# Kernel optimization log

Measured on AMD Instinct MI355X. Metric: run time of the kernel, lower is better.

Reference implementation:

```python
import jax, jax.numpy as jnp
import numpy as np

B, T, C, R = 4, 2048, 2048, 256


def setup_inputs() -> dict:
    key = jax.random.key(0)
    ks = jax.random.split(key, 12)
    s = 0.02
    return {
        "x": jax.random.normal(ks[0], (B, T, C), dtype=jnp.float32),
        "h_state": jnp.zeros((B, C), dtype=jnp.float32),
        "ln_gamma": jnp.ones((C,), dtype=jnp.float32),
        "ln_beta": jnp.zeros((C,), dtype=jnp.float32),
        "wq_a": jax.random.normal(ks[1], (C, R), dtype=jnp.float32) * s,
        "wq_b": jax.random.normal(ks[2], (R, C), dtype=jnp.float32) * s,
        "wk_a": jax.random.normal(ks[3], (C, R), dtype=jnp.float32) * s,
        "wk_b": jax.random.normal(ks[4], (R, C), dtype=jnp.float32) * s,
        "wv_a": jax.random.normal(ks[5], (C, R), dtype=jnp.float32) * s,
        "wv_b": jax.random.normal(ks[6], (R, C), dtype=jnp.float32) * s,
        "out_w": jax.random.normal(ks[7], (C, C), dtype=jnp.float32) * s,
        "out_b": jnp.zeros((C,), dtype=jnp.float32),
        "time_decay": jnp.full((C,), -0.5, dtype=jnp.float32),
    }


def _layernorm(x, gamma, beta, eps=1e-5):
    mu = jnp.mean(x, axis=-1, keepdims=True)
    var = jnp.var(x, axis=-1, keepdims=True)
    return (x - mu) * jax.lax.rsqrt(var + eps) * gamma + beta


def reference(x, h_state, ln_gamma, ln_beta, wq_a, wq_b, wk_a, wk_b, wv_a, wv_b, out_w, out_b, time_decay):
    b, t, c = x.shape
    xn = _layernorm(x, ln_gamma, ln_beta)
    # token shift: mix current with previous token
    x_shift = jnp.concatenate([jnp.zeros((b, 1, c), xn.dtype), xn[:, :-1, :]], axis=1)
    mix = 0.5 * xn + 0.5 * x_shift
    # low-rank projections: (B,T,C) @ (C,R) @ (R,C)
    q = jnp.einsum('btc,cr,rd->btd', mix, wq_a, wq_b)
    k = jnp.einsum('btc,cr,rd->btd', mix, wk_a, wk_b)
    v = jnp.einsum('btc,cr,rd->btd', mix, wv_a, wv_b)
    decay = jnp.exp(-jnp.exp(time_decay))  # (C,)

    kv = (k * v).transpose(1, 0, 2)          # (T,B,C)
    sq = jax.nn.sigmoid(q).transpose(1, 0, 2)  # (T,B,C)

    def step(h, inp):
        kv_t, sq_t = inp
        h = decay * h + kv_t
        return h, sq_t * h

    h_final, ys = jax.lax.scan(step, h_state, (kv, sq))
    out = ys.transpose(1, 0, 2)               # (B,T,C)
    out = jnp.einsum('btc,dc->btd', out, out_w) + out_b
    return out, h_final
```

## Files before the change

### kernel.cpp

```cpp
#include <hip/hip_runtime.h>


typedef __attribute__((ext_vector_type(8))) __bf16 bf16x8;
typedef __attribute__((ext_vector_type(4))) float f32x4;

static constexpr int Bb = 4, Tt = 2048, Cc = 2048, Rr = 256;
static constexpr int Mrows = Bb * Tt;
static constexpr int NCH = 32, CLEN = 64;

__device__ __forceinline__ unsigned short f2bf(float f) {
  union { float f; unsigned u; } a; a.f = f;
  unsigned r = (a.u + 0x7FFFu + ((a.u >> 16) & 1u)) >> 16;
  return (unsigned short)r;
}
__device__ __forceinline__ float bf2f(unsigned short h) {
  union { unsigned u; float f; } a; a.u = ((unsigned)h) << 16;
  return a.f;
}

__device__ __forceinline__ void gload16(const void* g, void* l) {
  __builtin_amdgcn_global_load_lds(
      (const __attribute__((address_space(1))) void*)g,
      (__attribute__((address_space(3))) void*)l, 16, 0, 0);
}

__global__ void prep_weights(const float* __restrict__ wqa, const float* __restrict__ wka,
                             const float* __restrict__ wva, const float* __restrict__ wqb,
                             const float* __restrict__ wkb, const float* __restrict__ wvb,
                             const float* __restrict__ ow,  const float* __restrict__ td,
                             unsigned short* __restrict__ waT, unsigned short* __restrict__ wbT,
                             unsigned short* __restrict__ owT, float* __restrict__ decay,
                             float* __restrict__ decayL) {
  const int g = blockIdx.x * blockDim.x + threadIdx.x;
  const int stride = gridDim.x * blockDim.x;
  for (int i = g; i < 3 * Rr * Cc; i += stride) {
    int c = i & (Cc - 1); int jj = i >> 11; int p = jj >> 8; int r = jj & (Rr - 1);
    const float* w = (p == 0) ? wqa : ((p == 1) ? wka : wva);
    waT[i] = f2bf(w[(size_t)c * Rr + r]);
  }
  for (int i = g; i < 3 * Cc * Rr; i += stride) {
    int r = i & (Rr - 1); int d = (i >> 8) & (Cc - 1); int p = i >> 19;
    const float* w = (p == 0) ? wqb : ((p == 1) ? wkb : wvb);
    wbT[i] = f2bf(w[(size_t)r * Cc + d]);
  }
  for (int i = g; i < Cc * Cc; i += stride) owT[i] = f2bf(ow[i]);
  for (int i = g; i < Cc; i += stride) {
    float e = expf(td[i]);
    decay[i] = expf(-e);
    decayL[i] = expf(-(float)CLEN * e);
  }
}

__global__ __launch_bounds__(256) void lnmix_kernel(
    const float* __restrict__ x, const float* __restrict__ gamma,
    const float* __restrict__ beta, unsigned short* __restrict__ mix) {
  const int m = blockIdx.x;
  const int t = m & (Tt - 1);
  const float* xr = x + (size_t)m * Cc;
  float s0 = 0.f, q0 = 0.f, s1 = 0.f, q1 = 0.f;
  float4 cur[2], prv[2];
#pragma unroll
  for (int r = 0; r < 2; ++r) {
    int i = threadIdx.x + r * 256;
    float4 v = ((const float4*)xr)[i];
    cur[r] = v;
    s0 += v.x + v.y + v.z + v.w;
    q0 += v.x * v.x + v.y * v.y + v.z * v.z + v.w * v.w;
  }
  if (t > 0) {
    const float* xp = xr - Cc;
#pragma unroll
    for (int r = 0; r < 2; ++r) {
      int i = threadIdx.x + r * 256;
      float4 v = ((const float4*)xp)[i];
      prv[r] = v;
      s1 += v.x + v.y + v.z + v.w;
      q1 += v.x * v.x + v.y * v.y + v.z * v.z + v.w * v.w;
    }
  }
#pragma unroll
  for (int off = 32; off; off >>= 1) {
    s0 += __shfl_down(s0, off); q0 += __shfl_down(q0, off);
    s1 += __shfl_down(s1, off); q1 += __shfl_down(q1, off);
  }
  __shared__ float red[4][4];
  __shared__ float bc[4];
  if ((threadIdx.x & 63) == 0) {
    int w = threadIdx.x >> 6;
    red[w][0] = s0; red[w][1] = q0; red[w][2] = s1; red[w][3] = q1;
  }
  __syncthreads();
  if (threadIdx.x == 0) {
    float a0 = 0, b0 = 0, a1 = 0, b1 = 0;
    for (int w = 0; w < 4; ++w) { a0 += red[w][0]; b0 += red[w][1]; a1 += red[w][2]; b1 += red[w][3]; }
    float mu0 = a0 * (1.f / Cc);
    bc[0] = mu0; bc[1] = rsqrtf(b0 * (1.f / Cc) - mu0 * mu0 + 1e-5f);
    float mu1 = a1 * (1.f / Cc);
    bc[2] = mu1; bc[3] = rsqrtf(b1 * (1.f / Cc) - mu1 * mu1 + 1e-5f);
  }
  __syncthreads();
  const float mu0 = bc[0], rs0 = bc[1], mu1 = bc[2], rs1 = bc[3];
#pragma unroll
  for (int r = 0; r < 2; ++r) {
    int i = threadIdx.x + r * 256;
    float4 g = ((const float4*)gamma)[i];
    float4 bb = ((const float4*)beta)[i];
    float4 v = cur[r];
    float mx = (v.x - mu0) * rs0 * g.x + bb.x;
    float my = (v.y - mu0) * rs0 * g.y + bb.y;
    float mz = (v.z - mu0) * rs0 * g.z + bb.z;
    float mw = (v.w - mu0) * rs0 * g.w + bb.w;
    if (t > 0) {
      float4 u = prv[r];
      mx = 0.5f * (mx + (u.x - mu1) * rs1 * g.x + bb.x);
      my = 0.5f * (my + (u.y - mu1) * rs1 * g.y + bb.y);
      mz = 0.5f * (mz + (u.z - mu1) * rs1 * g.z + bb.z);
      mw = 0.5f * (mw + (u.w - mu1) * rs1 * g.w + bb.w);
    } else {
      mx *= 0.5f; my *= 0.5f; mz *= 0.5f; mw *= 0.5f;
    }
    ushort4 o;
    o.x = f2bf(mx); o.y = f2bf(my); o.z = f2bf(mz); o.w = f2bf(mw);
    ((ushort4*)mix)[(size_t)m * 512 + i] = o;
  }
}

template <bool STORE_BF16, bool ADD_BIAS>
__global__ __launch_bounds__(512, 2) void gemm_pipe(
    const unsigned short* __restrict__ A0p, long lda, long aStrideP,
    const unsigned short* __restrict__ B0p, long ldb, long bStrideP,
    void* c0, void* c1, void* c2, long ldc, int K,
    const float* __restrict__ bias, int nbx, int nby) {
  __shared__ unsigned short lds[4 * 16384];
  const int tid = threadIdx.x;
  const int nwg = gridDim.x;
  const int id = blockIdx.x;
  const int q = nwg >> 3;
  const int swz = (id & 7) * q + (id >> 3);
  const int per = nbx * nby;
  const int p = swz / per;
  const int r2 = swz - p * per;
  const int mblk = r2 / nbx;
  const int nblk = r2 - mblk * nbx;
  const unsigned short* A  = A0p + (long)p * aStrideP;
  const unsigned short* Bt = B0p + (long)p * bStrideP;
  void* Cout = (p == 0) ? c0 : (p == 1 ? c1 : c2);
  const long m0 = (long)mblk * 256, n0 = (long)nblk * 256;

  const int lane = tid & 63, wid = tid >> 6;
  const int wm = wid >> 2, wn = wid & 3;
  const int fr = lane & 15, fq = lane >> 4;

  const int srow = tid >> 2;
  const int s_src = (tid & 3) ^ ((tid >> 3) & 3);
  const unsigned short* Ag = A + (m0 + srow) * lda + s_src * 8;
  const unsigned short* Bg = Bt + (n0 + srow) * ldb + s_src * 8;

  const int swzs = fq ^ ((fr >> 1) & 3);
  const unsigned short* aBase = &lds[(wm * 128 + fr) * 32 + swzs * 8];
  const unsigned short* bBase = &lds[8192 + (wn * 64 + fr) * 32 + swzs * 8];

  f32x4 acc[8][4];
#pragma unroll
  for (int i = 0; i < 8; ++i)
#pragma unroll
    for (int j = 0; j < 4; ++j) acc[i][j] = (f32x4){0.f, 0.f, 0.f, 0.f};

  const int NT = K >> 5;

  auto stageA = [&](int t) {
    unsigned short* d = &lds[(t & 3) * 16384 + tid * 8];
    const long kt = (long)t * 32;
    gload16(Ag + kt, d);
    gload16(Ag + 128 * lda + kt, d + 4096);
  };
  auto stageB = [&](int t) {
    unsigned short* d = &lds[(t & 3) * 16384 + 8192 + tid * 8];
    const long kt = (long)t * 32;
    gload16(Bg + kt, d);
    gload16(Bg + 128 * ldb + kt, d + 4096);
  };

  stageA(0); stageB(0);
  stageA(1); stageB(1);
  stageA(2); stageB(2);

  for (int t = 0; t < NT; ++t) {
    const int rem = NT - 1 - t;
    if (rem >= 2)      asm volatile("s_waitcnt vmcnt(8)" ::: "memory");
    else if (rem == 1) asm volatile("s_waitcnt vmcnt(4)" ::: "memory");
    else               asm volatile("s_waitcnt vmcnt(0)" ::: "memory");
    __builtin_amdgcn_s_barrier();
    __builtin_amdgcn_sched_barrier(0);

    const unsigned short* ab = aBase + (t & 3) * 16384;
    const unsigned short* bb = bBase + (t & 3) * 16384;

    bf16x8 bf[4], af[8];
#pragma unroll
    for (int j = 0; j < 4; ++j) bf[j] = *(const bf16x8*)(bb + j * 512);
#pragma unroll
    for (int i = 0; i < 8; ++i) af[i] = *(const bf16x8*)(ab + i * 512);
    if (t + 3 < NT) { stageA(t + 3); stageB(t + 3); }
    __builtin_amdgcn_s_setprio(1);
#pragma unroll
    for (int i = 0; i < 8; ++i)
#pragma unroll
      for (int j = 0; j < 4; ++j)
        acc[i][j] = __builtin_amdgcn_mfma_f32_16x16x32_bf16(af[i], bf[j], acc[i][j], 0, 0, 0);
    __builtin_amdgcn_s_setprio(0);
  }

#pragma unroll
  for (int j = 0; j < 4; ++j) {
    const long col = n0 + wn * 64 + j * 16 + fr;
    const float bv = ADD_BIAS ? bias[col] : 0.0f;
#pragma unroll
    for (int i = 0; i < 8; ++i) {
      const long row0 = m0 + wm * 128 + i * 16 + fq * 4;
#pragma unroll
      for (int r = 0; r < 4; ++r) {
        float val = acc[i][j][r] + bv;
        if (STORE_BF16)
          ((unsigned short*)Cout)[(row0 + r) * ldc + col] = f2bf(val);
        else
          ((float*)Cout)[(row0 + r) * ldc + col] = val;
      }
    }
  }
}

__global__ void addcvt_kernel(const float* __restrict__ p0, const float* __restrict__ p1,
                              unsigned short* __restrict__ o, int n4) {
  for (int i = blockIdx.x * blockDim.x + threadIdx.x; i < n4; i += gridDim.x * blockDim.x) {
    float4 a = ((const float4*)p0)[i];
    float4 b = ((const float4*)p1)[i];
    ushort4 r;
    r.x = f2bf(a.x + b.x); r.y = f2bf(a.y + b.y);
    r.z = f2bf(a.z + b.z); r.w = f2bf(a.w + b.w);
    ((ushort4*)o)[i] = r;
  }
}

__global__ void scan_phaseA(const unsigned short* __restrict__ k, const unsigned short* __restrict__ v,
                            const float* __restrict__ decay, float* __restrict__ hend) {
  const int g = blockIdx.x * 256 + threadIdx.x;
  const int c = g & (Cc - 1);
  const int j = (g >> 11) & (NCH - 1);
  const int b = g >> 16;
  const float d = decay[c];
  size_t base = ((size_t)(b * Tt + j * CLEN)) * Cc + c;
  float h = 0.f;
#pragma unroll 8
  for (int s = 0; s < CLEN; ++s) {
    size_t idx = base + (size_t)s * Cc;
    float kv = bf2f(k[idx]) * bf2f(v[idx]);
    h = fmaf(d, h, kv);
  }
  hend[(size_t)(b * NCH + j) * Cc + c] = h;
}

__global__ void scan_combine(const float* __restrict__ hend, const float* __restrict__ h0,
                             const float* __restrict__ decayL, float* __restrict__ Hin,
                             float* __restrict__ hfinal) {
  const int g = blockIdx.x * 256 + threadIdx.x;
  const int c = g & (Cc - 1);
  float H = h0[g];
  const float dl = decayL[c];
  const int b = g >> 11;
  for (int j = 0; j < NCH; ++j) {
    size_t idx = (size_t)(b * NCH + j) * Cc + c;
    Hin[idx] = H;
    H = fmaf(dl, H, hend[idx]);
  }
  hfinal[g] = H;
}

__global__ void scan_phaseB(const unsigned short* __restrict__ q, const unsigned short* __restrict__ k,
                            const unsigned short* __restrict__ v, const float* __restrict__ decay,
                            const float* __restrict__ Hin, unsigned short* __restrict__ ys) {
  const int g = blockIdx.x * 256 + threadIdx.x;
  const int c = g & (Cc - 1);
  const int j = (g >> 11) & (NCH - 1);
  const int b = g >> 16;
  const float d = decay[c];
  float h = Hin[(size_t)(b * NCH + j) * Cc + c];
  size_t base = ((size_t)(b * Tt + j * CLEN)) * Cc + c;
#pragma unroll 4
  for (int s = 0; s < CLEN; ++s) {
    size_t idx = base + (size_t)s * Cc;
    float kv = bf2f(k[idx]) * bf2f(v[idx]);
    h = fmaf(d, h, kv);
    float qq = bf2f(q[idx]);
    float sg = 1.f / (1.f + expf(-qq));
    ys[idx] = f2bf(sg * h);
  }
}

extern "C" void kernel_launch(void* const* d_in, const int* in_sizes, int n_in,
                              void* d_out, int out_size, void* d_ws, size_t ws_size,
                              hipStream_t stream) {
  const float* x   = (const float*)d_in[0];
  const float* h0  = (const float*)d_in[1];
  const float* gam = (const float*)d_in[2];
  const float* bet = (const float*)d_in[3];
  const float* wqa = (const float*)d_in[4];
  const float* wqb = (const float*)d_in[5];
  const float* wka = (const float*)d_in[6];
  const float* wkb = (const float*)d_in[7];
  const float* wva = (const float*)d_in[8];
  const float* wvb = (const float*)d_in[9];
  const float* ow  = (const float*)d_in[10];
  const float* ob  = (const float*)d_in[11];
  const float* td  = (const float*)d_in[12];
  float* out = (float*)d_out;

  char* ws = (char*)d_ws;
  unsigned short* waT   = (unsigned short*)(ws + 0);
  unsigned short* wbT   = (unsigned short*)(ws + 3145728);
  unsigned short* owT   = (unsigned short*)(ws + 6291456);
  float*          decay = (float*)(ws + 14680064);
  float*          decayL= (float*)(ws + 14688256);
  unsigned short* mixb  = (unsigned short*)(ws + 14761984);
  unsigned short* tmp   = (unsigned short*)(ws + 48316416);
  unsigned short* vp    = (unsigned short*)(ws + 60899328);
  float*          hend  = (float*)(ws + 94453760);
  float*          Hin   = (float*)(ws + 95502336);
  float* P0 = (float*)d_out;
  float* P1 = P0 + (size_t)Mrows * 768;
  unsigned short* qp = (unsigned short*)d_out;
  unsigned short* kp = qp + (size_t)Mrows * Cc;
  float* hfinal = out + (size_t)Mrows * Cc;
  unsigned short* ysb = mixb;

  prep_weights<<<1024, 256, 0, stream>>>(wqa, wka, wva, wqb, wkb, wvb, ow, td,
                                         waT, wbT, owT, decay, decayL);
  lnmix_kernel<<<Mrows, 256, 0, stream>>>(x, gam, bet, mixb);

  gemm_pipe<false, false><<<192, 512, 0, stream>>>(
      mixb, Cc, 1024, waT, Cc, 1024,
      P0, P1, nullptr, 768, 1024, nullptr, 3, 32);
  addcvt_kernel<<<1024, 256, 0, stream>>>(P0, P1, tmp, Mrows * 768 / 4);

  gemm_pipe<true, false><<<8 * 32 * 3, 512, 0, stream>>>(
      tmp, 768, 256, wbT, Rr, (long)Cc * Rr,
      qp, kp, vp, Cc, Rr, nullptr, 8, 32);

  scan_phaseA<<<(Bb * NCH * Cc) / 256, 256, 0, stream>>>(kp, vp, decay, hend);
  scan_combine<<<(Bb * Cc) / 256, 256, 0, stream>>>(hend, h0, decayL, Hin, hfinal);
  scan_phaseB<<<(Bb * NCH * Cc) / 256, 256, 0, stream>>>(qp, kp, vp, decay, Hin, ysb);

  gemm_pipe<false, true><<<8 * 32, 512, 0, stream>>>(
      ysb, Cc, 0, owT, Cc, 0,
      out, out, out, Cc, Cc, ob, 8, 32);
}
```

Before: 255.2 us.

## Load GEMM B operand directly into registers and deepen A LDS pipeline

The GEMM kernel stops staging the B tile through LDS. Each wave now loads its B fragments from global memory straight into registers, double-buffered across pairs of k-steps. The freed LDS is used for eight A stages instead of four, and the block-to-tile mapping is changed to iterate m fastest within n. This removes LDS traffic and ds_reads for B, but it makes B global loads less shared across waves, adds register pressure, and relies on a single vmcnt(8) wait whose counts must match the mixed global-to-LDS and register loads.

```diff
diff --git a/kernel.cpp b/kernel.cpp
--- a/kernel.cpp
+++ b/kernel.cpp
@@ -131,7 +131,7 @@
     const unsigned short* __restrict__ B0p, long ldb, long bStrideP,
     void* c0, void* c1, void* c2, long ldc, int K,
     const float* __restrict__ bias, int nbx, int nby) {
-  __shared__ unsigned short lds[4 * 16384];
+  __shared__ unsigned short lds[8 * 8192];
   const int tid = threadIdx.x;
   const int nwg = gridDim.x;
   const int id = blockIdx.x;
@@ -140,8 +140,8 @@
   const int per = nbx * nby;
   const int p = swz / per;
   const int r2 = swz - p * per;
-  const int mblk = r2 / nbx;
-  const int nblk = r2 - mblk * nbx;
+  const int nblk = r2 / nby;
+  const int mblk = r2 - nblk * nby;
   const unsigned short* A  = A0p + (long)p * aStrideP;
   const unsigned short* Bt = B0p + (long)p * bStrideP;
   void* Cout = (p == 0) ? c0 : (p == 1 ? c1 : c2);
@@ -154,11 +154,11 @@
   const int srow = tid >> 2;
   const int s_src = (tid & 3) ^ ((tid >> 3) & 3);
   const unsigned short* Ag = A + (m0 + srow) * lda + s_src * 8;
-  const unsigned short* Bg = Bt + (n0 + srow) * ldb + s_src * 8;
 
   const int swzs = fq ^ ((fr >> 1) & 3);
   const unsigned short* aBase = &lds[(wm * 128 + fr) * 32 + swzs * 8];
-  const unsigned short* bBase = &lds[8192 + (wn * 64 + fr) * 32 + swzs * 8];
+
+  const unsigned short* Bgp = Bt + (n0 + wn * 64 + fr) * ldb + fq * 8;
 
   f32x4 acc[8][4];
 #pragma unroll
@@ -167,48 +167,60 @@
     for (int j = 0; j < 4; ++j) acc[i][j] = (f32x4){0.f, 0.f, 0.f, 0.f};
 
   const int NT = K >> 5;
+  const int NP = NT >> 1;
 
   auto stageA = [&](int t) {
-    unsigned short* d = &lds[(t & 3) * 16384 + tid * 8];
+    unsigned short* d = &lds[(t & 7) * 8192 + tid * 8];
     const long kt = (long)t * 32;
     gload16(Ag + kt, d);
     gload16(Ag + 128 * lda + kt, d + 4096);
   };
-  auto stageB = [&](int t) {
-    unsigned short* d = &lds[(t & 3) * 16384 + 8192 + tid * 8];
-    const long kt = (long)t * 32;
-    gload16(Bg + kt, d);
-    gload16(Bg + 128 * ldb + kt, d + 4096);
+  bf16x8 bcur[4], bnxt[4];
+  auto loadB = [&](bf16x8* dst, int t) {
+    const long co = (long)t * 32;
+#pragma unroll
+    for (int j = 0; j < 4; ++j)
+      dst[j] = *(const bf16x8*)(Bgp + (long)(j * 16) * ldb + co);
   };
 
-  stageA(0); stageB(0);
-  stageA(1); stageB(1);
-  stageA(2); stageB(2);
-
-  for (int t = 0; t < NT; ++t) {
-    const int rem = NT - 1 - t;
-    if (rem >= 2)      asm volatile("s_waitcnt vmcnt(8)" ::: "memory");
-    else if (rem == 1) asm volatile("s_waitcnt vmcnt(4)" ::: "memory");
-    else               asm volatile("s_waitcnt vmcnt(0)" ::: "memory");
+  stageA(0); stageA(1); stageA(2); stageA(3);
+  loadB(bcur, 0);
+
+  for (int pr = 0; pr < NP; ++pr) {
+    const int t0 = 2 * pr, t1 = 2 * pr + 1;
+    asm volatile("s_waitcnt vmcnt(8)" ::: "memory");
     __builtin_amdgcn_s_barrier();
     __builtin_amdgcn_sched_barrier(0);
 
-    const unsigned short* ab = aBase + (t & 3) * 16384;
-    const unsigned short* bb = bBase + (t & 3) * 16384;
-
-    bf16x8 bf[4], af[8];
-#pragma unroll
-    for (int j = 0; j < 4; ++j) bf[j] = *(const bf16x8*)(bb + j * 512);
-#pragma unroll
-    for (int i = 0; i < 8; ++i) af[i] = *(const bf16x8*)(ab + i * 512);
-    if (t + 3 < NT) { stageA(t + 3); stageB(t + 3); }
-    __builtin_amdgcn_s_setprio(1);
-#pragma unroll
-    for (int i = 0; i < 8; ++i)
-#pragma unroll
-      for (int j = 0; j < 4; ++j)
-        acc[i][j] = __builtin_amdgcn_mfma_f32_16x16x32_bf16(af[i], bf[j], acc[i][j], 0, 0, 0);
-    __builtin_amdgcn_s_setprio(0);
+    {
+      const unsigned short* ab = aBase + (t0 & 7) * 8192;
+      bf16x8 af[8];
+#pragma unroll
+      for (int i = 0; i < 8; ++i) af[i] = *(const bf16x8*)(ab + i * 512);
+      loadB(bnxt, t1);
+      if (t0 + 4 < NT) { stageA(t0 + 4); stageA(t0 + 5); }
+      __builtin_amdgcn_s_setprio(1);
+#pragma unroll
+      for (int i = 0; i < 8; ++i)
+#pragma unroll
+        for (int j = 0; j < 4; ++j)
+          acc[i][j] = __builtin_amdgcn_mfma_f32_16x16x32_bf16(af[i], bcur[j], acc[i][j], 0, 0, 0);
+      __builtin_amdgcn_s_setprio(0);
+    }
+    {
+      const unsigned short* ab = aBase + (t1 & 7) * 8192;
+      bf16x8 af[8];
+#pragma unroll
+      for (int i = 0; i < 8; ++i) af[i] = *(const bf16x8*)(ab + i * 512);
+      if (t1 + 1 < NT) loadB(bcur, t1 + 1);
+      __builtin_amdgcn_s_setprio(1);
+#pragma unroll
+      for (int i = 0; i < 8; ++i)
+#pragma unroll
+        for (int j = 0; j < 4; ++j)
+          acc[i][j] = __builtin_amdgcn_mfma_f32_16x16x32_bf16(af[i], bnxt[j], acc[i][j], 0, 0, 0);
+      __builtin_amdgcn_s_setprio(0);
+    }
   }
 
 #pragma unroll
```

New measurement: 300.2 us. 17.6% more time.

## Shrink GEMM tile to 256x128 with 256 threads and triple-buffered LDS

Applied to the files above, without the earlier changes.

Changes the GEMM workgroup from 512 threads and a 256x256 tile to 256 threads and a 256x128 tile, doubling the grid sizes so more workgroups are available to fill the GPU. The LDS pipeline goes from four stages to three with a smaller per-stage footprint, and the load prefetch depth drops from 3 to 2. The aim is better occupancy and load balance, especially for the small 192- and 256-block launches. The cost is less data reuse per tile (more global/L2 traffic for A) and a shallower prefetch that may expose memory latency.

```diff
diff --git a/kernel.cpp b/kernel.cpp
--- a/kernel.cpp
+++ b/kernel.cpp
@@ -126,12 +126,12 @@
 }
 
 template <bool STORE_BF16, bool ADD_BIAS>
-__global__ __launch_bounds__(512, 2) void gemm_pipe(
+__global__ __launch_bounds__(256, 2) void gemm_pipe(
     const unsigned short* __restrict__ A0p, long lda, long aStrideP,
     const unsigned short* __restrict__ B0p, long ldb, long bStrideP,
     void* c0, void* c1, void* c2, long ldc, int K,
     const float* __restrict__ bias, int nbx, int nby) {
-  __shared__ unsigned short lds[4 * 16384];
+  __shared__ unsigned short lds[3 * 12288];
   const int tid = threadIdx.x;
   const int nwg = gridDim.x;
   const int id = blockIdx.x;
@@ -145,10 +145,10 @@
   const unsigned short* A  = A0p + (long)p * aStrideP;
   const unsigned short* Bt = B0p + (long)p * bStrideP;
   void* Cout = (p == 0) ? c0 : (p == 1 ? c1 : c2);
-  const long m0 = (long)mblk * 256, n0 = (long)nblk * 256;
+  const long m0 = (long)mblk * 256, n0 = (long)nblk * 128;
 
   const int lane = tid & 63, wid = tid >> 6;
-  const int wm = wid >> 2, wn = wid & 3;
+  const int wm = wid >> 1, wn = wid & 1;
   const int fr = lane & 15, fq = lane >> 4;
 
   const int srow = tid >> 2;
@@ -168,40 +168,36 @@
 
   const int NT = K >> 5;
 
-  auto stageA = [&](int t) {
-    unsigned short* d = &lds[(t & 3) * 16384 + tid * 8];
+  auto stage = [&](int t, int buf) {
+    unsigned short* dA = &lds[buf * 12288 + tid * 8];
+    unsigned short* dB = &lds[buf * 12288 + 8192 + tid * 8];
     const long kt = (long)t * 32;
-    gload16(Ag + kt, d);
-    gload16(Ag + 128 * lda + kt, d + 4096);
+#pragma unroll
+    for (int l = 0; l < 4; ++l)
+      gload16(Ag + (long)(l * 64) * lda + kt, dA + l * 2048);
+#pragma unroll
+    for (int l = 0; l < 2; ++l)
+      gload16(Bg + (long)(l * 64) * ldb + kt, dB + l * 2048);
   };
-  auto stageB = [&](int t) {
-    unsigned short* d = &lds[(t & 3) * 16384 + 8192 + tid * 8];
-    const long kt = (long)t * 32;
-    gload16(Bg + kt, d);
-    gload16(Bg + 128 * ldb + kt, d + 4096);
-  };
-
-  stageA(0); stageB(0);
-  stageA(1); stageB(1);
-  stageA(2); stageB(2);
+
+  stage(0, 0); stage(1, 1);
+  int bufR = 0, bufS = 2;
 
   for (int t = 0; t < NT; ++t) {
-    const int rem = NT - 1 - t;
-    if (rem >= 2)      asm volatile("s_waitcnt vmcnt(8)" ::: "memory");
-    else if (rem == 1) asm volatile("s_waitcnt vmcnt(4)" ::: "memory");
-    else               asm volatile("s_waitcnt vmcnt(0)" ::: "memory");
+    if (t < NT - 1) asm volatile("s_waitcnt vmcnt(6)" ::: "memory");
+    else            asm volatile("s_waitcnt vmcnt(0)" ::: "memory");
     __builtin_amdgcn_s_barrier();
     __builtin_amdgcn_sched_barrier(0);
 
-    const unsigned short* ab = aBase + (t & 3) * 16384;
-    const unsigned short* bb = bBase + (t & 3) * 16384;
+    const unsigned short* ab = aBase + bufR * 12288;
+    const unsigned short* bb = bBase + bufR * 12288;
 
     bf16x8 bf[4], af[8];
 #pragma unroll
     for (int j = 0; j < 4; ++j) bf[j] = *(const bf16x8*)(bb + j * 512);
 #pragma unroll
     for (int i = 0; i < 8; ++i) af[i] = *(const bf16x8*)(ab + i * 512);
-    if (t + 3 < NT) { stageA(t + 3); stageB(t + 3); }
+    if (t + 2 < NT) stage(t + 2, bufS);
     __builtin_amdgcn_s_setprio(1);
 #pragma unroll
     for (int i = 0; i < 8; ++i)
@@ -209,6 +205,9 @@
       for (int j = 0; j < 4; ++j)
         acc[i][j] = __builtin_amdgcn_mfma_f32_16x16x32_bf16(af[i], bf[j], acc[i][j], 0, 0, 0);
     __builtin_amdgcn_s_setprio(0);
+
+    bufR = (bufR == 2) ? 0 : bufR + 1;
+    bufS = (bufS == 2) ? 0 : bufS + 1;
   }
 
 #pragma unroll
@@ -337,20 +336,20 @@
                                          waT, wbT, owT, decay, decayL);
   lnmix_kernel<<<Mrows, 256, 0, stream>>>(x, gam, bet, mixb);
 
-  gemm_pipe<false, false><<<192, 512, 0, stream>>>(
+  gemm_pipe<false, false><<<384, 256, 0, stream>>>(
       mixb, Cc, 1024, waT, Cc, 1024,
-      P0, P1, nullptr, 768, 1024, nullptr, 3, 32);
+      P0, P1, nullptr, 768, 1024, nullptr, 6, 32);
   addcvt_kernel<<<1024, 256, 0, stream>>>(P0, P1, tmp, Mrows * 768 / 4);
 
-  gemm_pipe<true, false><<<8 * 32 * 3, 512, 0, stream>>>(
+  gemm_pipe<true, false><<<1536, 256, 0, stream>>>(
       tmp, 768, 256, wbT, Rr, (long)Cc * Rr,
-      qp, kp, vp, Cc, Rr, nullptr, 8, 32);
+      qp, kp, vp, Cc, Rr, nullptr, 16, 32);
 
   scan_phaseA<<<(Bb * NCH * Cc) / 256, 256, 0, stream>>>(kp, vp, decay, hend);
   scan_combine<<<(Bb * Cc) / 256, 256, 0, stream>>>(hend, h0, decayL, Hin, hfinal);
   scan_phaseB<<<(Bb * NCH * Cc) / 256, 256, 0, stream>>>(qp, kp, vp, decay, Hin, ysb);
 
-  gemm_pipe<false, true><<<8 * 32, 512, 0, stream>>>(
+  gemm_pipe<false, true><<<512, 256, 0, stream>>>(
       ysb, Cc, 0, owT, Cc, 0,
-      out, out, out, Cc, Cc, ob, 8, 32);
-}
+      out, out, out, Cc, Cc, ob, 16, 32);
+}
```

Result: faster. 244.5 us (-4.2%).

## Loop each GEMM block over multiple problems with continuous cross-problem prefetch

Applied to the files above, without the earlier changes.

The GEMM kernel now lets one workgroup process several problems in sequence (q, k, v up-projections), keeping the 3-deep LDS prefetch pipeline running across problem boundaries and writing results out between them. The second GEMM launches 256 blocks that each handle three problems instead of 768 short blocks, which removes repeated pipeline prologue and drain costs and wave-quantization tails. Staging is moved ahead of the LDS fragment reads inside the loop, and launch bounds change from 2 to 1 blocks per CU. This may lower occupancy, and writing C in the middle of the loop can stall the pipeline.

```diff
diff --git a/kernel.cpp b/kernel.cpp
--- a/kernel.cpp
+++ b/kernel.cpp
@@ -126,10 +126,10 @@
 }
 
 template <bool STORE_BF16, bool ADD_BIAS>
-__global__ __launch_bounds__(512, 2) void gemm_pipe(
-    const unsigned short* __restrict__ A0p, long lda, long aStrideP,
-    const unsigned short* __restrict__ B0p, long ldb, long bStrideP,
-    void* c0, void* c1, void* c2, long ldc, int K,
+__global__ __launch_bounds__(512, 1) void gemm_mp(
+    const unsigned short* __restrict__ A0, long lda, long aStrideP,
+    const unsigned short* __restrict__ B0, long ldb, long bStrideP,
+    void* c0, void* c1, void* c2, long ldc, int NT2, int npLoop,
     const float* __restrict__ bias, int nbx, int nby) {
   __shared__ unsigned short lds[4 * 16384];
   const int tid = threadIdx.x;
@@ -138,13 +138,13 @@
   const int q = nwg >> 3;
   const int swz = (id & 7) * q + (id >> 3);
   const int per = nbx * nby;
-  const int p = swz / per;
-  const int r2 = swz - p * per;
+  const int pgrid = swz / per;
+  const int r2 = swz - pgrid * per;
   const int mblk = r2 / nbx;
   const int nblk = r2 - mblk * nbx;
-  const unsigned short* A  = A0p + (long)p * aStrideP;
-  const unsigned short* Bt = B0p + (long)p * bStrideP;
-  void* Cout = (p == 0) ? c0 : (p == 1 ? c1 : c2);
+  const int pgBase = pgrid * npLoop;
+  const unsigned short* A  = A0 + (long)pgBase * aStrideP;
+  const unsigned short* Bt = B0 + (long)pgBase * bStrideP;
   const long m0 = (long)mblk * 256, n0 = (long)nblk * 256;
 
   const int lane = tid & 63, wid = tid >> 6;
@@ -166,42 +166,67 @@
 #pragma unroll
     for (int j = 0; j < 4; ++j) acc[i][j] = (f32x4){0.f, 0.f, 0.f, 0.f};
 
-  const int NT = K >> 5;
-
-  auto stageA = [&](int t) {
-    unsigned short* d = &lds[(t & 3) * 16384 + tid * 8];
-    const long kt = (long)t * 32;
-    gload16(Ag + kt, d);
-    gload16(Ag + 128 * lda + kt, d + 4096);
+  const int TT = NT2 * npLoop;
+  const long KEL = (long)NT2 * 32;
+
+  auto stage = [&](long aOff, long bOff, int buf) {
+    unsigned short* dA = &lds[buf * 16384 + tid * 8];
+    unsigned short* dB = &lds[buf * 16384 + 8192 + tid * 8];
+    gload16(Ag + aOff, dA);
+    gload16(Ag + 128 * lda + aOff, dA + 4096);
+    gload16(Bg + bOff, dB);
+    gload16(Bg + 128 * ldb + bOff, dB + 4096);
   };
-  auto stageB = [&](int t) {
-    unsigned short* d = &lds[(t & 3) * 16384 + 8192 + tid * 8];
-    const long kt = (long)t * 32;
-    gload16(Bg + kt, d);
-    gload16(Bg + 128 * ldb + kt, d + 4096);
+
+  auto writeC = [&](int pe) {
+    void* Cp = (pe == 0) ? c0 : (pe == 1 ? c1 : c2);
+#pragma unroll
+    for (int j = 0; j < 4; ++j) {
+      const long col = n0 + wn * 64 + j * 16 + fr;
+      const float bv = ADD_BIAS ? bias[col] : 0.0f;
+#pragma unroll
+      for (int i = 0; i < 8; ++i) {
+        const long row0 = m0 + wm * 128 + i * 16 + fq * 4;
+#pragma unroll
+        for (int r = 0; r < 4; ++r) {
+          float val = acc[i][j][r] + bv;
+          if (STORE_BF16)
+            ((unsigned short*)Cp)[(row0 + r) * ldc + col] = f2bf(val);
+          else
+            ((float*)Cp)[(row0 + r) * ldc + col] = val;
+        }
+      }
+    }
   };
 
-  stageA(0); stageB(0);
-  stageA(1); stageB(1);
-  stageA(2); stageB(2);
-
-  for (int t = 0; t < NT; ++t) {
-    const int rem = NT - 1 - t;
+  stage(0, 0, 0);
+  stage(32, 32, 1);
+  stage(64, 64, 2);
+  long saOff = 96, sbOff = 96;
+  long skc = 96;
+  int rk = 0, rp = 0;
+
+  for (int t = 0; t < TT; ++t) {
+    const int rem = TT - 1 - t;
     if (rem >= 2)      asm volatile("s_waitcnt vmcnt(8)" ::: "memory");
     else if (rem == 1) asm volatile("s_waitcnt vmcnt(4)" ::: "memory");
     else               asm volatile("s_waitcnt vmcnt(0)" ::: "memory");
     __builtin_amdgcn_s_barrier();
     __builtin_amdgcn_sched_barrier(0);
 
+    if (t + 3 < TT) {
+      stage(saOff, sbOff, (t + 3) & 3);
+      saOff += 32; sbOff += 32; skc += 32;
+      if (skc == KEL) { skc = 0; saOff += aStrideP - KEL; sbOff += bStrideP - KEL; }
+    }
+
     const unsigned short* ab = aBase + (t & 3) * 16384;
     const unsigned short* bb = bBase + (t & 3) * 16384;
-
     bf16x8 bf[4], af[8];
 #pragma unroll
     for (int j = 0; j < 4; ++j) bf[j] = *(const bf16x8*)(bb + j * 512);
 #pragma unroll
     for (int i = 0; i < 8; ++i) af[i] = *(const bf16x8*)(ab + i * 512);
-    if (t + 3 < NT) { stageA(t + 3); stageB(t + 3); }
     __builtin_amdgcn_s_setprio(1);
 #pragma unroll
     for (int i = 0; i < 8; ++i)
@@ -209,22 +234,16 @@
       for (int j = 0; j < 4; ++j)
         acc[i][j] = __builtin_amdgcn_mfma_f32_16x16x32_bf16(af[i], bf[j], acc[i][j], 0, 0, 0);
     __builtin_amdgcn_s_setprio(0);
-  }
-
-#pragma unroll
-  for (int j = 0; j < 4; ++j) {
-    const long col = n0 + wn * 64 + j * 16 + fr;
-    const float bv = ADD_BIAS ? bias[col] : 0.0f;
-#pragma unroll
-    for (int i = 0; i < 8; ++i) {
-      const long row0 = m0 + wm * 128 + i * 16 + fq * 4;
-#pragma unroll
-      for (int r = 0; r < 4; ++r) {
-        float val = acc[i][j][r] + bv;
-        if (STORE_BF16)
-          ((unsigned short*)Cout)[(row0 + r) * ldc + col] = f2bf(val);
-        else
-          ((float*)Cout)[(row0 + r) * ldc + col] = val;
+
+    if (++rk == NT2) {
+      rk = 0;
+      writeC(pgBase + rp);
+      ++rp;
+      if (rp < npLoop) {
+#pragma unroll
+        for (int i = 0; i < 8; ++i)
+#pragma unroll
+          for (int j = 0; j < 4; ++j) acc[i][j] = (f32x4){0.f, 0.f, 0.f, 0.f};
       }
     }
   }
@@ -337,20 +356,20 @@
                                          waT, wbT, owT, decay, decayL);
   lnmix_kernel<<<Mrows, 256, 0, stream>>>(x, gam, bet, mixb);
 
-  gemm_pipe<false, false><<<192, 512, 0, stream>>>(
+  gemm_mp<false, false><<<192, 512, 0, stream>>>(
       mixb, Cc, 1024, waT, Cc, 1024,
-      P0, P1, nullptr, 768, 1024, nullptr, 3, 32);
+      P0, P1, nullptr, 768, 32, 1, nullptr, 3, 32);
   addcvt_kernel<<<1024, 256, 0, stream>>>(P0, P1, tmp, Mrows * 768 / 4);
 
-  gemm_pipe<true, false><<<8 * 32 * 3, 512, 0, stream>>>(
+  gemm_mp<true, false><<<256, 512, 0, stream>>>(
       tmp, 768, 256, wbT, Rr, (long)Cc * Rr,
-      qp, kp, vp, Cc, Rr, nullptr, 8, 32);
+      qp, kp, vp, Cc, 8, 3, nullptr, 8, 32);
 
   scan_phaseA<<<(Bb * NCH * Cc) / 256, 256, 0, stream>>>(kp, vp, decay, hend);
   scan_combine<<<(Bb * Cc) / 256, 256, 0, stream>>>(hend, h0, decayL, Hin, hfinal);
   scan_phaseB<<<(Bb * NCH * Cc) / 256, 256, 0, stream>>>(qp, kp, vp, decay, Hin, ysb);
 
-  gemm_pipe<false, true><<<8 * 32, 512, 0, stream>>>(
+  gemm_mp<false, true><<<256, 512, 0, stream>>>(
       ysb, Cc, 0, owT, Cc, 0,
-      out, out, out, Cc, Cc, ob, 8, 32);
-}
+      out, out, out, Cc, 64, 1, ob, 8, 32);
+}
```

New measurement: 261.7 us. 1.03x slower.
